# Optimization experiments

Hardware: AMD Instinct MI355X
Metric: run time of the kernel (lower is better)

The kernel has to match this reference:

```python
import jax, jax.numpy as jnp
import numpy as np

NUM_LAYERS = 2
HIDDEN = 512


def setup_inputs() -> dict:
    key = jax.random.key(0)
    ks = jax.random.split(key, 5)
    B, T, D, L, H = 32, 512, 512, NUM_LAYERS, HIDDEN
    s = 1.0 / np.sqrt(H)
    return {
        "x": jax.random.normal(ks[0], (B, T, D), dtype=jnp.float32),
        "h0": jnp.zeros((B, L, H), dtype=jnp.float32),
        "c0": jnp.zeros((B, L, H), dtype=jnp.float32),
        "Wx": jax.random.normal(ks[1], (L, 4 * H, D), dtype=jnp.float32) * s,
        "bx": jax.random.normal(ks[2], (L, 4 * H), dtype=jnp.float32) * s,
        "Wh": jax.random.normal(ks[3], (L, 4 * H, H), dtype=jnp.float32) * s,
        "bh": jax.random.normal(ks[4], (L, 4 * H), dtype=jnp.float32) * s,
    }


def _lstm_forward(x, h0, c0, Wx, bx, Wh, bh):
    # x: [B,T,D]; h0,c0: [B,L,H]; Wx/Wh: [L,4H,*]; gate order (i,f,g,o)
    L, H = Wx.shape[0], Wx.shape[2]

    def step(carry, x_t):
        h, c = carry  # [B,L,H]
        inp = x_t  # [B,D]
        new_h, new_c = [], []
        for l in range(L):
            gates = (inp @ Wx[l].T + bx[l]) + (h[:, l] @ Wh[l].T + bh[l])  # [B,4H]
            i_g, f_g, g_g, o_g = jnp.split(gates, 4, axis=-1)
            c_l = jax.nn.sigmoid(f_g) * c[:, l] + jax.nn.sigmoid(i_g) * jnp.tanh(g_g)
            h_l = jax.nn.sigmoid(o_g) * jnp.tanh(c_l)
            new_h.append(h_l)
            new_c.append(c_l)
            inp = h_l
        return (jnp.stack(new_h, axis=1), jnp.stack(new_c, axis=1)), inp

    (h_n, c_n), ys = jax.lax.scan(step, (h0, c0), jnp.swapaxes(x, 0, 1))
    output = jnp.swapaxes(ys, 0, 1)  # [B,T,H]
    # torch module returns h_n/c_n swapped to [num_layers, batch, hidden]
    return output, (jnp.swapaxes(h_n, 0, 1), jnp.swapaxes(c_n, 0, 1))


def reference(x, h0, c0, Wx, bx, Wh, bh):
    return _lstm_forward(x, h0, c0, Wx, bx, Wh, bh)
```

## Files before the change

kernel.cpp:

```cpp
#include <hip/hip_runtime.h>
#include <hip/hip_bf16.h>

typedef __bf16 bf16x8 __attribute__((ext_vector_type(8)));
typedef float f32x4 __attribute__((ext_vector_type(4)));
typedef unsigned long long u64;

#define MFMA16(a, b, c) __builtin_amdgcn_mfma_f32_16x16x32_bf16((a), (b), (c), 0, 0, 0)

#define HN_OFF 8388608ull
#define CN_OFF 8421376ull

__device__ __forceinline__ float sigf(float x) { return 1.0f / (1.0f + __expf(-x)); }
__device__ __forceinline__ float b2f(unsigned short u) {
    union { unsigned u; float f; } c; c.u = ((unsigned)u) << 16; return c.f;
}
__device__ __forceinline__ unsigned short f2u(float f) {
    __hip_bfloat16 h = __float2bfloat16(f); return *(unsigned short*)&h;
}

__device__ __forceinline__ u64 gload8(const void* p) {
    return __hip_atomic_load((const u64*)p, __ATOMIC_RELAXED, __HIP_MEMORY_SCOPE_AGENT);
}
__device__ __forceinline__ void gstore4(void* p, unsigned v) {
    __hip_atomic_store((unsigned*)p, v, __ATOMIC_RELAXED, __HIP_MEMORY_SCOPE_AGENT);
}

__device__ __forceinline__ void split8(const float* p, bf16x8& hi, bf16x8& lo) {
    union { __hip_bfloat16 h[8]; bf16x8 v; } uh, ul;
    #pragma unroll
    for (int i = 0; i < 8; ++i) {
        __hip_bfloat16 e = __float2bfloat16(p[i]);
        uh.h[i] = e;
        ul.h[i] = __float2bfloat16(p[i] - __bfloat162float(e));
    }
    hi = uh.v; lo = ul.v;
}

__global__ __launch_bounds__(256) void lstm_detect(
    const unsigned* __restrict__ Wq, unsigned* __restrict__ dflag,
    unsigned* __restrict__ flags)
{
    for (int j = threadIdx.x; j < 1024; j += 256) flags[j] = 0;
    if (threadIdx.x < 64) {
        int lane = threadIdx.x;
        int bad = 0;
        #pragma unroll
        for (int i = 0; i < 4; ++i) {
            unsigned u = Wq[(size_t)(lane + i * 64) * 4093];
            float v = b2f((unsigned short)(u & 0xFFFFu));
            if (!(v == v) || fabsf(v) > 100.0f) ++bad;
        }
        #pragma unroll
        for (int off = 32; off; off >>= 1) bad += __shfl_down(bad, off, 64);
        if (lane == 0) *dflag = (bad > 32) ? 1u : 0u;
    }
}

__global__ __launch_bounds__(256) void lstm_init(
    const void* __restrict__ h0v, const void* __restrict__ c0v,
    __hip_bfloat16* __restrict__ h0hi, __hip_bfloat16* __restrict__ h0lo,
    __hip_bfloat16* __restrict__ h1hi, __hip_bfloat16* __restrict__ h1lo,
    float* __restrict__ cws, const unsigned* __restrict__ dflag)
{
    const bool f32 = (*dflag != 0);
    int i = blockIdx.x * 256 + threadIdx.x;
    int b = i >> 9, n = i & 511;
    float f0, f1, g0, g1;
    if (f32) {
        const float* h = (const float*)h0v; const float* c = (const float*)c0v;
        f0 = h[(b * 2 + 0) * 512 + n];  f1 = h[(b * 2 + 1) * 512 + n];
        g0 = c[(b * 2 + 0) * 512 + n];  g1 = c[(b * 2 + 1) * 512 + n];
    } else {
        const unsigned short* h = (const unsigned short*)h0v;
        const unsigned short* c = (const unsigned short*)c0v;
        f0 = b2f(h[(b * 2 + 0) * 512 + n]);  f1 = b2f(h[(b * 2 + 1) * 512 + n]);
        g0 = b2f(c[(b * 2 + 0) * 512 + n]);  g1 = b2f(c[(b * 2 + 1) * 512 + n]);
    }
    __hip_bfloat16 e0 = __float2bfloat16(f0), e1 = __float2bfloat16(f1);
    h0hi[i] = e0; h0lo[i] = __float2bfloat16(f0 - __bfloat162float(e0));
    h1hi[i] = e1; h1lo[i] = __float2bfloat16(f1 - __bfloat162float(e1));
    cws[i] = g0;  cws[16384 + i] = g1;
}

__global__ __launch_bounds__(256, 1) void lstm_seq(
    const void* __restrict__ xv,
    const void* __restrict__ Wxv, const void* __restrict__ bxv,
    const void* __restrict__ Whv, const void* __restrict__ bhv,
    __hip_bfloat16* __restrict__ h0hi, __hip_bfloat16* __restrict__ h0lo,
    __hip_bfloat16* __restrict__ h1hi, __hip_bfloat16* __restrict__ h1lo,
    const float* __restrict__ cws, unsigned* __restrict__ flags,
    const unsigned* __restrict__ dflag, void* __restrict__ outv)
{
    const bool f32 = (*dflag != 0);
    const int p  = blockIdx.x & 1;
    const int wt = blockIdx.x >> 1;
    const int tid = threadIdx.x;
    const int q = tid >> 6, lane = tid & 63;
    const int n16 = lane & 15, quad = lane >> 4;
    const int colg = q * 512 + wt * 16 + n16;

    __shared__ __align__(16) char smem[131072];
    __shared__ float gbuf[2176];

    float* outf = (float*)outv;
    __hip_bfloat16* outh = (__hip_bfloat16*)outv;

    bf16x8 wa[16], wal[16], wr[16], wrl[16];
    if (f32) {
        const float* WA = (const float*)Wxv + ((size_t)(p * 2048 + colg)) * 512;
        const float* WR = (const float*)Whv + ((size_t)(p * 2048 + colg)) * 512;
        #pragma unroll
        for (int kk = 0; kk < 16; ++kk) {
            split8(WA + kk * 32 + quad * 8, wa[kk], wal[kk]);
            split8(WR + kk * 32 + quad * 8, wr[kk], wrl[kk]);
        }
    } else {
        const unsigned short* WA = (const unsigned short*)Wxv + ((size_t)(p * 2048 + colg)) * 512;
        const unsigned short* WR = (const unsigned short*)Whv + ((size_t)(p * 2048 + colg)) * 512;
        union { uint4 u; bf16x8 v; } cvu;
        #pragma unroll
        for (int kk = 0; kk < 16; ++kk) {
            cvu.u = *(const uint4*)(WA + kk * 32 + quad * 8); wa[kk] = cvu.v;
            cvu.u = *(const uint4*)(WR + kk * 32 + quad * 8); wr[kk] = cvu.v;
        }
    }
    float bias;
    if (f32) bias = ((const float*)bxv)[p * 2048 + colg] + ((const float*)bhv)[p * 2048 + colg];
    else     bias = b2f(((const unsigned short*)bxv)[p * 2048 + colg])
                  + b2f(((const unsigned short*)bhv)[p * 2048 + colg]);

    const int e0 = tid * 2;
    const int pbb = e0 >> 4;
    const int pn0 = e0 & 15;
    float cv[2];
    cv[0] = cws[p * 16384 + pbb * 512 + wt * 16 + pn0];
    cv[1] = cws[p * 16384 + pbb * 512 + wt * 16 + pn0 + 1];

    const unsigned short* xb = (const unsigned short*)xv;

    #define STAGE_X_BF16(T)                                                      \
        { _Pragma("unroll")                                                      \
          for (int j = 0; j < 8; ++j) {                                          \
              int L = j * 256 + tid;                                             \
              int rem = L & 127;                                                 \
              int row = ((rem >> 6) << 4) + (rem & 15);                          \
              int kcol = ((L >> 7) << 5) + (((rem >> 4) & 3) << 3);              \
              *(uint4*)(smem + (L << 4)) =                                       \
                  *(const uint4*)(xb + ((size_t)row * 512 + (T)) * 512 + kcol);  \
          } }

    #define STAGE_X_F32(T)                                                       \
        { _Pragma("unroll")                                                      \
          for (int j = 0; j < 8; ++j) {                                          \
              int L = j * 256 + tid;                                             \
              int rem = L & 127;                                                 \
              int row = ((rem >> 6) << 4) + (rem & 15);                          \
              int kcol = ((L >> 7) << 5) + (((rem >> 4) & 3) << 3);              \
              const float* xp = (const float*)xv + ((size_t)row * 512 + (T)) * 512 + kcol; \
              bf16x8 hi_, lo_;                                                   \
              split8(xp, hi_, lo_);                                              \
              *(bf16x8*)(smem + (L << 4)) = hi_;                                 \
              *(bf16x8*)(smem + 32768 + (L << 4)) = lo_;                         \
          } }

    #define GATHER2(SH, SL, DH, DL)                                              \
        { u64 vH[16], vL[16];                                                    \
          _Pragma("unroll")                                                      \
          for (int j = 0; j < 8; ++j) {                                          \
              int L = j * 256 + tid;                                             \
              int rem = L & 127;                                                 \
              int row = ((rem >> 6) << 4) + (rem & 15);                          \
              int kcol = ((L >> 7) << 5) + (((rem >> 4) & 3) << 3);              \
              size_t hoff = (size_t)row * 512 + kcol;                            \
              vH[j*2] = gload8((SH) + hoff); vH[j*2+1] = gload8((SH) + hoff + 4);\
              vL[j*2] = gload8((SL) + hoff); vL[j*2+1] = gload8((SL) + hoff + 4);\
          }                                                                      \
          _Pragma("unroll")                                                      \
          for (int j = 0; j < 8; ++j) {                                          \
              int L = j * 256 + tid;                                             \
              u64* dH = (u64*)(smem + (DH) + (L << 4));                          \
              u64* dL = (u64*)(smem + (DL) + (L << 4));                          \
              dH[0] = vH[j*2]; dH[1] = vH[j*2+1];                                \
              dL[0] = vL[j*2]; dL[1] = vL[j*2+1];                                \
          } }

    #define POLL(THR_E, THR_O)                                                   \
        { if (tid < 64) {                                                        \
              int thr_ = ((tid & 1) == 0) ? (THR_E) : (THR_O);                   \
              if (thr_ > 0) {                                                    \
                  while ((int)__hip_atomic_load(&flags[tid * 16],                \
                             __ATOMIC_RELAXED, __HIP_MEMORY_SCOPE_AGENT) < thr_) \
                      __builtin_amdgcn_s_sleep(1);                               \
              }                                                                  \
          }                                                                      \
          __syncthreads(); }

    #define MM_A_F32()                                                           \
        { _Pragma("unroll")                                                      \
          for (int kk = 0; kk < 16; ++kk) {                                      \
              bf16x8 Aha = *(const bf16x8*)(sl + kk * 2048);                     \
              bf16x8 Ahb = *(const bf16x8*)(sl + kk * 2048 + 1024);              \
              bf16x8 Ala = *(const bf16x8*)(sl + 32768 + kk * 2048);             \
              bf16x8 Alb = *(const bf16x8*)(sl + 32768 + kk * 2048 + 1024);      \
              acc0 = MFMA16(Aha, wa[kk], acc0);  acc1 = MFMA16(Ahb, wa[kk], acc1);   \
              acc0 = MFMA16(Aha, wal[kk], acc0); acc1 = MFMA16(Ahb, wal[kk], acc1);  \
              acc0 = MFMA16(Ala, wa[kk], acc0);  acc1 = MFMA16(Alb, wa[kk], acc1);   \
          } }

    #define MM_R_F32()                                                           \
        { _Pragma("unroll")                                                      \
          for (int kk = 0; kk < 16; ++kk) {                                      \
              bf16x8 Rha = *(const bf16x8*)(sl + 65536 + kk * 2048);             \
              bf16x8 Rhb = *(const bf16x8*)(sl + 65536 + kk * 2048 + 1024);      \
              bf16x8 Rla = *(const bf16x8*)(sl + 98304 + kk * 2048);             \
              bf16x8 Rlb = *(const bf16x8*)(sl + 98304 + kk * 2048 + 1024);      \
              acc0 = MFMA16(Rha, wr[kk], acc0);  acc1 = MFMA16(Rhb, wr[kk], acc1);   \
              acc0 = MFMA16(Rha, wrl[kk], acc0); acc1 = MFMA16(Rhb, wrl[kk], acc1);  \
              acc0 = MFMA16(Rla, wr[kk], acc0);  acc1 = MFMA16(Rlb, wr[kk], acc1);   \
          } }

    #define MM_A_BF16_P0()                                                       \
        { _Pragma("unroll")                                                      \
          for (int kk = 0; kk < 16; ++kk) {                                      \
              bf16x8 Aha = *(const bf16x8*)(sl + kk * 2048);                     \
              bf16x8 Ahb = *(const bf16x8*)(sl + kk * 2048 + 1024);              \
              acc0 = MFMA16(Aha, wa[kk], acc0);  acc1 = MFMA16(Ahb, wa[kk], acc1);   \
          } }

    #define MM_A_BF16_P1()                                                       \
        { _Pragma("unroll")                                                      \
          for (int kk = 0; kk < 16; ++kk) {                                      \
              bf16x8 Aha = *(const bf16x8*)(sl + kk * 2048);                     \
              bf16x8 Ahb = *(const bf16x8*)(sl + kk * 2048 + 1024);              \
              bf16x8 Ala = *(const bf16x8*)(sl + 32768 + kk * 2048);             \
              bf16x8 Alb = *(const bf16x8*)(sl + 32768 + kk * 2048 + 1024);      \
              acc0 = MFMA16(Aha, wa[kk], acc0);  acc1 = MFMA16(Ahb, wa[kk], acc1);   \
              acc0 = MFMA16(Ala, wa[kk], acc0);  acc1 = MFMA16(Alb, wa[kk], acc1);   \
          } }

    #define MM_R_BF16()                                                          \
        { _Pragma("unroll")                                                      \
          for (int kk = 0; kk < 16; ++kk) {                                      \
              bf16x8 Rha = *(const bf16x8*)(sl + 65536 + kk * 2048);             \
              bf16x8 Rhb = *(const bf16x8*)(sl + 65536 + kk * 2048 + 1024);      \
              bf16x8 Rla = *(const bf16x8*)(sl + 98304 + kk * 2048);             \
              bf16x8 Rlb = *(const bf16x8*)(sl + 98304 + kk * 2048 + 1024);      \
              acc0 = MFMA16(Rha, wr[kk], acc0);  acc1 = MFMA16(Rhb, wr[kk], acc1);   \
              acc0 = MFMA16(Rla, wr[kk], acc0);  acc1 = MFMA16(Rlb, wr[kk], acc1);   \
          } }

    if (p == 0) {
        if (f32) { STAGE_X_F32(0) } else { STAGE_X_BF16(0) }
        __syncthreads();
    }

    for (int k = 0; k <= 512; ++k) {
        const bool doComp = (p == 0) ? (k < 512) : (k > 0);
        if (!doComp) {
            if (tid == 0)
                __hip_atomic_store(&flags[blockIdx.x * 16], (unsigned)(k + 1),
                                   __ATOMIC_RELAXED, __HIP_MEMORY_SCOPE_AGENT);
            continue;
        }

        const char* sl = smem + (lane << 4);
        f32x4 acc0 = {bias, bias, bias, bias};
        f32x4 acc1 = {bias, bias, bias, bias};
        const int t = (p == 0) ? k : (k - 1);

        if (p == 0) {
            if (f32) { MM_A_F32() } else { MM_A_BF16_P0() }
            POLL(k, k - 2)
            {
                const __hip_bfloat16* Rhi = h0hi + (size_t)(k & 3) * 16384;
                const __hip_bfloat16* Rlo = h0lo + (size_t)(k & 3) * 16384;
                GATHER2(Rhi, Rlo, 65536, 98304)
            }
            __syncthreads();
            if (f32) { MM_R_F32() } else { MM_R_BF16() }
        } else {
            POLL(k, 0)
            {
                const __hip_bfloat16* Ahi = h0hi + (size_t)(k & 3) * 16384;
                const __hip_bfloat16* Alo = h0lo + (size_t)(k & 3) * 16384;
                GATHER2(Ahi, Alo, 0, 32768)
            }
            __syncthreads();
            if (f32) { MM_A_F32() } else { MM_A_BF16_P1() }
            POLL(0, k)
            {
                const __hip_bfloat16* Rhi = h1hi + (size_t)((k + 1) & 1) * 16384;
                const __hip_bfloat16* Rlo = h1lo + (size_t)((k + 1) & 1) * 16384;
                GATHER2(Rhi, Rlo, 65536, 98304)
            }
            __syncthreads();
            if (f32) { MM_R_F32() } else { MM_R_BF16() }
        }

        #pragma unroll
        for (int r = 0; r < 4; ++r) {
            gbuf[(q * 32 + quad * 4 + r) * 17 + n16]      = acc0[r];
            gbuf[(q * 32 + 16 + quad * 4 + r) * 17 + n16] = acc1[r];
        }
        __syncthreads();

        __hip_bfloat16* Ohi = (p == 0) ? h0hi + (size_t)((k + 1) & 3) * 16384
                                       : h1hi + (size_t)(k & 1) * 16384;
        __hip_bfloat16* Olo = (p == 0) ? h0lo + (size_t)((k + 1) & 3) * 16384
                                       : h1lo + (size_t)(k & 1) * 16384;
        float rh[2], rc[2];
        #pragma unroll
        for (int j = 0; j < 2; ++j) {
            int n = pn0 + j;
            float ig = gbuf[(0 * 32 + pbb) * 17 + n];
            float fg = gbuf[(1 * 32 + pbb) * 17 + n];
            float gg = gbuf[(2 * 32 + pbb) * 17 + n];
            float og = gbuf[(3 * 32 + pbb) * 17 + n];
            float cnew = sigf(fg) * cv[j] + sigf(ig) * tanhf(gg);
            cv[j] = cnew;
            rc[j] = cnew;
            rh[j] = sigf(og) * tanhf(cnew);
        }
        unsigned phi = 0, plo = 0, pcn = 0;
        #pragma unroll
        for (int j = 0; j < 2; ++j) {
            unsigned short hu = f2u(rh[j]);
            unsigned short lu = f2u(rh[j] - b2f(hu));
            phi |= ((unsigned)hu) << (16 * j);
            plo |= ((unsigned)lu) << (16 * j);
            pcn |= ((unsigned)f2u(rc[j])) << (16 * j);
        }
        const int idx = pbb * 512 + wt * 16 + pn0;
        gstore4(Ohi + idx, phi);
        gstore4(Olo + idx, plo);

        __syncthreads();
        if (tid == 0)
            __hip_atomic_store(&flags[blockIdx.x * 16], (unsigned)(k + 1),
                               __ATOMIC_RELAXED, __HIP_MEMORY_SCOPE_AGENT);

        if (p == 1) {
            size_t oidx = ((size_t)pbb * 512 + t) * 512 + wt * 16 + pn0;
            if (f32) { outf[oidx] = rh[0]; outf[oidx + 1] = rh[1]; }
            else     { *(unsigned*)(outh + oidx) = phi; }
            if (k == 512) {
                if (f32) {
                    outf[HN_OFF + 16384 + idx] = rh[0]; outf[HN_OFF + 16385 + idx] = rh[1];
                    outf[CN_OFF + 16384 + idx] = rc[0]; outf[CN_OFF + 16385 + idx] = rc[1];
                } else {
                    *(unsigned*)(outh + HN_OFF + 16384 + idx) = phi;
                    *(unsigned*)(outh + CN_OFF + 16384 + idx) = pcn;
                }
            }
        } else if (k == 511) {
            if (f32) {
                outf[HN_OFF + idx] = rh[0]; outf[HN_OFF + idx + 1] = rh[1];
                outf[CN_OFF + idx] = rc[0]; outf[CN_OFF + idx + 1] = rc[1];
            } else {
                *(unsigned*)(outh + HN_OFF + idx) = phi;
                *(unsigned*)(outh + CN_OFF + idx) = pcn;
            }
        }

        if (p == 0) {
            if (k + 1 < 512) {
                if (f32) { STAGE_X_F32(k + 1) } else { STAGE_X_BF16(k + 1) }
            }
            __syncthreads();
        }
    }
}

extern "C" void kernel_launch(void* const* d_in, const int* in_sizes, int n_in,
                              void* d_out, int out_size, void* d_ws, size_t ws_size,
                              hipStream_t stream)
{
    const void* x  = d_in[0];
    const void* h0 = d_in[1];
    const void* c0 = d_in[2];
    const void* Wx = d_in[3];
    const void* bx = d_in[4];
    const void* Wh = d_in[5];
    const void* bh = d_in[6];

    char* ws = (char*)d_ws;
    __hip_bfloat16* h0hi = (__hip_bfloat16*)(ws);
    __hip_bfloat16* h0lo = (__hip_bfloat16*)(ws + 131072);
    __hip_bfloat16* h1hi = (__hip_bfloat16*)(ws + 262144);
    __hip_bfloat16* h1lo = (__hip_bfloat16*)(ws + 327680);
    float*          cws  = (float*)(ws + 393216);
    unsigned*       flags = (unsigned*)(ws + 524288);
    unsigned*       dflag = (unsigned*)(ws + 528384);

    lstm_detect<<<1, 256, 0, stream>>>((const unsigned*)Wx, dflag, flags);
    lstm_init<<<64, 256, 0, stream>>>(h0, c0, h0hi, h0lo, h1hi, h1lo, cws, dflag);
    lstm_seq<<<64, 256, 0, stream>>>(x, Wx, bx, Wh, bh,
                                     h0hi, h0lo, h1hi, h1lo, cws, flags, dflag, d_out);
}
```

Measured before the change: 6.215 ms.

## Embed step tags in packed hidden-state words to replace flag polling

Packs each hidden value's bf16 hi part and truncated lo part into one 32-bit word, with a 4-bit step tag in the low bits of the lo part. Consumers issue the gather loads first and spin until every tag matches, so readiness is checked on the data itself instead of polling per-block flags and then gathering. Layer-0 blocks only wait on a loose flag bound set by layer-1 blocks, to avoid overwriting buffers still in use. This is meant to remove one synchronization round-trip per step from the critical path of the recurrence. The cost is 4 fewer bits of precision in the lo correction term, plus repeated wide reloads whenever a tag check fails.

```diff
diff --git a/kernel.cpp b/kernel.cpp
--- a/kernel.cpp
+++ b/kernel.cpp
@@ -21,8 +21,8 @@
 __device__ __forceinline__ u64 gload8(const void* p) {
     return __hip_atomic_load((const u64*)p, __ATOMIC_RELAXED, __HIP_MEMORY_SCOPE_AGENT);
 }
-__device__ __forceinline__ void gstore4(void* p, unsigned v) {
-    __hip_atomic_store((unsigned*)p, v, __ATOMIC_RELAXED, __HIP_MEMORY_SCOPE_AGENT);
+__device__ __forceinline__ void gstore8(void* p, u64 v) {
+    __hip_atomic_store((u64*)p, v, __ATOMIC_RELAXED, __HIP_MEMORY_SCOPE_AGENT);
 }
 
 __device__ __forceinline__ void split8(const float* p, bf16x8& hi, bf16x8& lo) {
@@ -58,8 +58,7 @@
 
 __global__ __launch_bounds__(256) void lstm_init(
     const void* __restrict__ h0v, const void* __restrict__ c0v,
-    __hip_bfloat16* __restrict__ h0hi, __hip_bfloat16* __restrict__ h0lo,
-    __hip_bfloat16* __restrict__ h1hi, __hip_bfloat16* __restrict__ h1lo,
+    unsigned* __restrict__ h0p, unsigned* __restrict__ h1p,
     float* __restrict__ cws, const unsigned* __restrict__ dflag)
 {
     const bool f32 = (*dflag != 0);
@@ -76,9 +75,10 @@
         f0 = b2f(h[(b * 2 + 0) * 512 + n]);  f1 = b2f(h[(b * 2 + 1) * 512 + n]);
         g0 = b2f(c[(b * 2 + 0) * 512 + n]);  g1 = b2f(c[(b * 2 + 1) * 512 + n]);
     }
-    __hip_bfloat16 e0 = __float2bfloat16(f0), e1 = __float2bfloat16(f1);
-    h0hi[i] = e0; h0lo[i] = __float2bfloat16(f0 - __bfloat162float(e0));
-    h1hi[i] = e1; h1lo[i] = __float2bfloat16(f1 - __bfloat162float(e1));
+    unsigned short h0h = f2u(f0), h1h = f2u(f1);
+    unsigned short h0l = f2u(f0 - b2f(h0h)), h1l = f2u(f1 - b2f(h1h));
+    h0p[i] = ((unsigned)h0h << 16) | ((unsigned)h0l & 0xFFF0u) | 15u;
+    h1p[i] = ((unsigned)h1h << 16) | ((unsigned)h1l & 0xFFF0u) | 0u;
     cws[i] = g0;  cws[16384 + i] = g1;
 }
 
@@ -86,8 +86,7 @@
     const void* __restrict__ xv,
     const void* __restrict__ Wxv, const void* __restrict__ bxv,
     const void* __restrict__ Whv, const void* __restrict__ bhv,
-    __hip_bfloat16* __restrict__ h0hi, __hip_bfloat16* __restrict__ h0lo,
-    __hip_bfloat16* __restrict__ h1hi, __hip_bfloat16* __restrict__ h1lo,
+    unsigned* __restrict__ h0p, unsigned* __restrict__ h1p,
     const float* __restrict__ cws, unsigned* __restrict__ flags,
     const unsigned* __restrict__ dflag, void* __restrict__ outv)
 {
@@ -163,37 +162,47 @@
               *(bf16x8*)(smem + 32768 + (L << 4)) = lo_;                         \
           } }
 
-    #define GATHER2(SH, SL, DH, DL)                                              \
-        { u64 vH[16], vL[16];                                                    \
-          _Pragma("unroll")                                                      \
-          for (int j = 0; j < 8; ++j) {                                          \
-              int L = j * 256 + tid;                                             \
-              int rem = L & 127;                                                 \
-              int row = ((rem >> 6) << 4) + (rem & 15);                          \
-              int kcol = ((L >> 7) << 5) + (((rem >> 4) & 3) << 3);              \
-              size_t hoff = (size_t)row * 512 + kcol;                            \
-              vH[j*2] = gload8((SH) + hoff); vH[j*2+1] = gload8((SH) + hoff + 4);\
-              vL[j*2] = gload8((SL) + hoff); vL[j*2+1] = gload8((SL) + hoff + 4);\
-          }                                                                      \
-          _Pragma("unroll")                                                      \
-          for (int j = 0; j < 8; ++j) {                                          \
-              int L = j * 256 + tid;                                             \
-              u64* dH = (u64*)(smem + (DH) + (L << 4));                          \
-              u64* dL = (u64*)(smem + (DL) + (L << 4));                          \
-              dH[0] = vH[j*2]; dH[1] = vH[j*2+1];                                \
-              dL[0] = vL[j*2]; dL[1] = vL[j*2+1];                                \
-          } }
-
-    #define POLL(THR_E, THR_O)                                                   \
-        { if (tid < 64) {                                                        \
-              int thr_ = ((tid & 1) == 0) ? (THR_E) : (THR_O);                   \
-              if (thr_ > 0) {                                                    \
-                  while ((int)__hip_atomic_load(&flags[tid * 16],                \
-                             __ATOMIC_RELAXED, __HIP_MEMORY_SCOPE_AGENT) < thr_) \
-                      __builtin_amdgcn_s_sleep(1);                               \
-              }                                                                  \
-          }                                                                      \
-          __syncthreads(); }
+    #define EOFF(S_) ({ int L_ = ((S_) >> 2) * 256 + tid; int rem_ = L_ & 127;    \
+        int row_ = ((rem_ >> 6) << 4) + (rem_ & 15);                              \
+        int kc_  = ((L_ >> 7) << 5) + (((rem_ >> 4) & 3) << 3);                   \
+        row_ * 512 + kc_ + ((S_) & 3) * 2; })
+
+    #define GISSUE(SRC)                                                           \
+        { _Pragma("unroll")                                                       \
+          for (int s_ = 0; s_ < 32; ++s_) V[s_] = gload8((const unsigned*)(SRC) + EOFF(s_)); }
+
+    #define GCHECK(SRC, WANTV)                                                    \
+        { const u64 WV_ = (u64)(WANTV) * 0x0000000100000001ULL;                   \
+          for (;;) {                                                              \
+              u64 d_ = 0;                                                         \
+              _Pragma("unroll")                                                   \
+              for (int s_ = 0; s_ < 32; ++s_)                                     \
+                  d_ |= (V[s_] ^ WV_) & 0x0000000F0000000FULL;                    \
+              if (d_ == 0) break;                                                 \
+              __builtin_amdgcn_s_sleep(1);                                        \
+              _Pragma("unroll")                                                   \
+              for (int s_ = 0; s_ < 32; ++s_)                                     \
+                  V[s_] = gload8((const unsigned*)(SRC) + EOFF(s_));              \
+          } }
+
+    #define GSCATTER(DH, DL)                                                      \
+        { _Pragma("unroll")                                                       \
+          for (int j_ = 0; j_ < 8; ++j_) {                                        \
+              union { u64 q; unsigned w[2]; } a_, b_, c_, d_;                     \
+              a_.q = V[j_*4+0]; b_.q = V[j_*4+1]; c_.q = V[j_*4+2]; d_.q = V[j_*4+3]; \
+              uint4 hi_, lo_;                                                     \
+              hi_.x = (a_.w[0] >> 16) | (a_.w[1] & 0xFFFF0000u);                  \
+              hi_.y = (b_.w[0] >> 16) | (b_.w[1] & 0xFFFF0000u);                  \
+              hi_.z = (c_.w[0] >> 16) | (c_.w[1] & 0xFFFF0000u);                  \
+              hi_.w = (d_.w[0] >> 16) | (d_.w[1] & 0xFFFF0000u);                  \
+              lo_.x = (a_.w[0] & 0xFFF0u) | ((a_.w[1] & 0xFFF0u) << 16);          \
+              lo_.y = (b_.w[0] & 0xFFF0u) | ((b_.w[1] & 0xFFF0u) << 16);          \
+              lo_.z = (c_.w[0] & 0xFFF0u) | ((c_.w[1] & 0xFFF0u) << 16);          \
+              lo_.w = (d_.w[0] & 0xFFF0u) | ((d_.w[1] & 0xFFF0u) << 16);          \
+              int L_ = j_ * 256 + tid;                                            \
+              *(uint4*)(smem + (DH) + (L_ << 4)) = hi_;                           \
+              *(uint4*)(smem + (DL) + (L_ << 4)) = lo_;                           \
+          } }
 
     #define MM_A_F32()                                                           \
         { _Pragma("unroll")                                                      \
@@ -249,101 +258,129 @@
               acc0 = MFMA16(Rla, wr[kk], acc0);  acc1 = MFMA16(Rlb, wr[kk], acc1);   \
           } }
 
+    #define EPILOGUE(ODST, TG)                                                    \
+        { _Pragma("unroll")                                                       \
+          for (int r = 0; r < 4; ++r) {                                           \
+              gbuf[(q * 32 + quad * 4 + r) * 17 + n16]      = acc0[r];            \
+              gbuf[(q * 32 + 16 + quad * 4 + r) * 17 + n16] = acc1[r];            \
+          } }
+
+    const char* sl = smem + (lane << 4);
+
     if (p == 0) {
         if (f32) { STAGE_X_F32(0) } else { STAGE_X_BF16(0) }
         __syncthreads();
-    }
-
-    for (int k = 0; k <= 512; ++k) {
-        const bool doComp = (p == 0) ? (k < 512) : (k > 0);
-        if (!doComp) {
+
+        for (int k = 0; k < 512; ++k) {
+            const unsigned want = (unsigned)((k - 1) & 15);
+            u64 V[32];
+            const unsigned* h0src = h0p + (size_t)(k & 3) * 16384;
+
+            GISSUE(h0src)
+            f32x4 acc0 = {bias, bias, bias, bias};
+            f32x4 acc1 = {bias, bias, bias, bias};
+            if (f32) { MM_A_F32() } else { MM_A_BF16_P0() }
+            GCHECK(h0src, want)
+            GSCATTER(65536, 98304)
+            __syncthreads();
+            if (f32) { MM_R_F32() } else { MM_R_BF16() }
+
+            EPILOGUE(,)
+            if (k >= 3 && tid < 32) {
+                while ((int)__hip_atomic_load(&flags[tid * 16],
+                           __ATOMIC_RELAXED, __HIP_MEMORY_SCOPE_AGENT) < k - 2)
+                    __builtin_amdgcn_s_sleep(2);
+            }
+            __syncthreads();
+
+            float rh[2], rc[2];
+            #pragma unroll
+            for (int j = 0; j < 2; ++j) {
+                int n = pn0 + j;
+                float ig = gbuf[(0 * 32 + pbb) * 17 + n];
+                float fg = gbuf[(1 * 32 + pbb) * 17 + n];
+                float gg = gbuf[(2 * 32 + pbb) * 17 + n];
+                float og = gbuf[(3 * 32 + pbb) * 17 + n];
+                float cnew = sigf(fg) * cv[j] + sigf(ig) * tanhf(gg);
+                cv[j] = cnew; rc[j] = cnew;
+                rh[j] = sigf(og) * tanhf(cnew);
+            }
+            const unsigned tg = (unsigned)(k & 15);
+            unsigned short hu0 = f2u(rh[0]), hu1 = f2u(rh[1]);
+            unsigned short lu0 = f2u(rh[0] - b2f(hu0)), lu1 = f2u(rh[1] - b2f(hu1));
+            unsigned w0 = ((unsigned)hu0 << 16) | ((unsigned)lu0 & 0xFFF0u) | tg;
+            unsigned w1 = ((unsigned)hu1 << 16) | ((unsigned)lu1 & 0xFFF0u) | tg;
+            const int idx = pbb * 512 + wt * 16 + pn0;
+            gstore8(h0p + (size_t)((k + 1) & 3) * 16384 + idx, ((u64)w1 << 32) | w0);
+
+            if (k == 511) {
+                unsigned phi = (unsigned)hu0 | ((unsigned)hu1 << 16);
+                unsigned pcn = (unsigned)f2u(rc[0]) | ((unsigned)f2u(rc[1]) << 16);
+                if (f32) {
+                    outf[HN_OFF + idx] = rh[0]; outf[HN_OFF + idx + 1] = rh[1];
+                    outf[CN_OFF + idx] = rc[0]; outf[CN_OFF + idx + 1] = rc[1];
+                } else {
+                    *(unsigned*)(outh + HN_OFF + idx) = phi;
+                    *(unsigned*)(outh + CN_OFF + idx) = pcn;
+                }
+            }
+            if (k + 1 < 512) { if (f32) { STAGE_X_F32(k + 1) } else { STAGE_X_BF16(k + 1) } }
+            __syncthreads();
+        }
+    } else {
+        for (int k = 1; k <= 512; ++k) {
+            const int t = k - 1;
+            const unsigned want = (unsigned)((k - 1) & 15);
+            u64 V[32];
+
+            const unsigned* h1src = h1p + (size_t)((k + 1) & 1) * 16384;
+            GISSUE(h1src)
+            GCHECK(h1src, want)
+            GSCATTER(65536, 98304)
+            __syncthreads();
+
+            const unsigned* h0src = h0p + (size_t)(k & 3) * 16384;
+            GISSUE(h0src)
+            f32x4 acc0 = {bias, bias, bias, bias};
+            f32x4 acc1 = {bias, bias, bias, bias};
+            if (f32) { MM_R_F32() } else { MM_R_BF16() }
+            GCHECK(h0src, want)
+            GSCATTER(0, 32768)
+            __syncthreads();
             if (tid == 0)
-                __hip_atomic_store(&flags[blockIdx.x * 16], (unsigned)(k + 1),
+                __hip_atomic_store(&flags[wt * 16], (unsigned)k,
                                    __ATOMIC_RELAXED, __HIP_MEMORY_SCOPE_AGENT);
-            continue;
-        }
-
-        const char* sl = smem + (lane << 4);
-        f32x4 acc0 = {bias, bias, bias, bias};
-        f32x4 acc1 = {bias, bias, bias, bias};
-        const int t = (p == 0) ? k : (k - 1);
-
-        if (p == 0) {
-            if (f32) { MM_A_F32() } else { MM_A_BF16_P0() }
-            POLL(k, k - 2)
-            {
-                const __hip_bfloat16* Rhi = h0hi + (size_t)(k & 3) * 16384;
-                const __hip_bfloat16* Rlo = h0lo + (size_t)(k & 3) * 16384;
-                GATHER2(Rhi, Rlo, 65536, 98304)
+            if (f32) { MM_A_F32() } else { MM_A_BF16_P1() }
+
+            EPILOGUE(,)
+            __syncthreads();
+
+            float rh[2], rc[2];
+            #pragma unroll
+            for (int j = 0; j < 2; ++j) {
+                int n = pn0 + j;
+                float ig = gbuf[(0 * 32 + pbb) * 17 + n];
+                float fg = gbuf[(1 * 32 + pbb) * 17 + n];
+                float gg = gbuf[(2 * 32 + pbb) * 17 + n];
+                float og = gbuf[(3 * 32 + pbb) * 17 + n];
+                float cnew = sigf(fg) * cv[j] + sigf(ig) * tanhf(gg);
+                cv[j] = cnew; rc[j] = cnew;
+                rh[j] = sigf(og) * tanhf(cnew);
             }
-            __syncthreads();
-            if (f32) { MM_R_F32() } else { MM_R_BF16() }
-        } else {
-            POLL(k, 0)
-            {
-                const __hip_bfloat16* Ahi = h0hi + (size_t)(k & 3) * 16384;
-                const __hip_bfloat16* Alo = h0lo + (size_t)(k & 3) * 16384;
-                GATHER2(Ahi, Alo, 0, 32768)
-            }
-            __syncthreads();
-            if (f32) { MM_A_F32() } else { MM_A_BF16_P1() }
-            POLL(0, k)
-            {
-                const __hip_bfloat16* Rhi = h1hi + (size_t)((k + 1) & 1) * 16384;
-                const __hip_bfloat16* Rlo = h1lo + (size_t)((k + 1) & 1) * 16384;
-                GATHER2(Rhi, Rlo, 65536, 98304)
-            }
-            __syncthreads();
-            if (f32) { MM_R_F32() } else { MM_R_BF16() }
-        }
-
-        #pragma unroll
-        for (int r = 0; r < 4; ++r) {
-            gbuf[(q * 32 + quad * 4 + r) * 17 + n16]      = acc0[r];
-            gbuf[(q * 32 + 16 + quad * 4 + r) * 17 + n16] = acc1[r];
-        }
-        __syncthreads();
-
-        __hip_bfloat16* Ohi = (p == 0) ? h0hi + (size_t)((k + 1) & 3) * 16384
-                                       : h1hi + (size_t)(k & 1) * 16384;
-        __hip_bfloat16* Olo = (p == 0) ? h0lo + (size_t)((k + 1) & 3) * 16384
-                                       : h1lo + (size_t)(k & 1) * 16384;
-        float rh[2], rc[2];
-        #pragma unroll
-        for (int j = 0; j < 2; ++j) {
-            int n = pn0 + j;
-            float ig = gbuf[(0 * 32 + pbb) * 17 + n];
-            float fg = gbuf[(1 * 32 + pbb) * 17 + n];
-            float gg = gbuf[(2 * 32 + pbb) * 17 + n];
-            float og = gbuf[(3 * 32 + pbb) * 17 + n];
-            float cnew = sigf(fg) * cv[j] + sigf(ig) * tanhf(gg);
-            cv[j] = cnew;
-            rc[j] = cnew;
-            rh[j] = sigf(og) * tanhf(cnew);
-        }
-        unsigned phi = 0, plo = 0, pcn = 0;
-        #pragma unroll
-        for (int j = 0; j < 2; ++j) {
-            unsigned short hu = f2u(rh[j]);
-            unsigned short lu = f2u(rh[j] - b2f(hu));
-            phi |= ((unsigned)hu) << (16 * j);
-            plo |= ((unsigned)lu) << (16 * j);
-            pcn |= ((unsigned)f2u(rc[j])) << (16 * j);
-        }
-        const int idx = pbb * 512 + wt * 16 + pn0;
-        gstore4(Ohi + idx, phi);
-        gstore4(Olo + idx, plo);
-
-        __syncthreads();
-        if (tid == 0)
-            __hip_atomic_store(&flags[blockIdx.x * 16], (unsigned)(k + 1),
-                               __ATOMIC_RELAXED, __HIP_MEMORY_SCOPE_AGENT);
-
-        if (p == 1) {
+            const unsigned tg = (unsigned)(k & 15);
+            unsigned short hu0 = f2u(rh[0]), hu1 = f2u(rh[1]);
+            unsigned short lu0 = f2u(rh[0] - b2f(hu0)), lu1 = f2u(rh[1] - b2f(hu1));
+            unsigned w0 = ((unsigned)hu0 << 16) | ((unsigned)lu0 & 0xFFF0u) | tg;
+            unsigned w1 = ((unsigned)hu1 << 16) | ((unsigned)lu1 & 0xFFF0u) | tg;
+            const int idx = pbb * 512 + wt * 16 + pn0;
+            gstore8(h1p + (size_t)(k & 1) * 16384 + idx, ((u64)w1 << 32) | w0);
+
+            unsigned phi = (unsigned)hu0 | ((unsigned)hu1 << 16);
             size_t oidx = ((size_t)pbb * 512 + t) * 512 + wt * 16 + pn0;
             if (f32) { outf[oidx] = rh[0]; outf[oidx + 1] = rh[1]; }
             else     { *(unsigned*)(outh + oidx) = phi; }
             if (k == 512) {
+                unsigned pcn = (unsigned)f2u(rc[0]) | ((unsigned)f2u(rc[1]) << 16);
                 if (f32) {
                     outf[HN_OFF + 16384 + idx] = rh[0]; outf[HN_OFF + 16385 + idx] = rh[1];
                     outf[CN_OFF + 16384 + idx] = rc[0]; outf[CN_OFF + 16385 + idx] = rc[1];
@@ -352,21 +389,6 @@
                     *(unsigned*)(outh + CN_OFF + 16384 + idx) = pcn;
                 }
             }
-        } else if (k == 511) {
-            if (f32) {
-                outf[HN_OFF + idx] = rh[0]; outf[HN_OFF + idx + 1] = rh[1];
-                outf[CN_OFF + idx] = rc[0]; outf[CN_OFF + idx + 1] = rc[1];
-            } else {
-                *(unsigned*)(outh + HN_OFF + idx) = phi;
-                *(unsigned*)(outh + CN_OFF + idx) = pcn;
-            }
-        }
-
-        if (p == 0) {
-            if (k + 1 < 512) {
-                if (f32) { STAGE_X_F32(k + 1) } else { STAGE_X_BF16(k + 1) }
-            }
-            __syncthreads();
         }
     }
 }
@@ -384,16 +406,14 @@
     const void* bh = d_in[6];
 
     char* ws = (char*)d_ws;
-    __hip_bfloat16* h0hi = (__hip_bfloat16*)(ws);
-    __hip_bfloat16* h0lo = (__hip_bfloat16*)(ws + 131072);
-    __hip_bfloat16* h1hi = (__hip_bfloat16*)(ws + 262144);
-    __hip_bfloat16* h1lo = (__hip_bfloat16*)(ws + 327680);
-    float*          cws  = (float*)(ws + 393216);
-    unsigned*       flags = (unsigned*)(ws + 524288);
-    unsigned*       dflag = (unsigned*)(ws + 528384);
+    unsigned* h0p  = (unsigned*)(ws);
+    unsigned* h1p  = (unsigned*)(ws + 262144);
+    float*    cws  = (float*)(ws + 393216);
+    unsigned* flags = (unsigned*)(ws + 524288);
+    unsigned* dflag = (unsigned*)(ws + 528384);
 
     lstm_detect<<<1, 256, 0, stream>>>((const unsigned*)Wx, dflag, flags);
-    lstm_init<<<64, 256, 0, stream>>>(h0, c0, h0hi, h0lo, h1hi, h1lo, cws, dflag);
+    lstm_init<<<64, 256, 0, stream>>>(h0, c0, h0p, h1p, cws, dflag);
     lstm_seq<<<64, 256, 0, stream>>>(x, Wx, bx, Wh, bh,
-                                     h0hi, h0lo, h1hi, h1lo, cws, flags, dflag, d_out);
-}
+                                     h0p, h1p, cws, flags, dflag, d_out);
+}
```

Result: slower. 7.190 ms (+15.7%).
